# Optimization experiments

Hardware: AMD Instinct MI355X
Metric: run time of the kernel (lower is better)

## Reference

```python
import jax, jax.numpy as jnp
import numpy as np

D = 256; H = 8; DK = 32; L = 5; FF = 2048; K = 31
EPS_LN = 1e-12  # espnet LayerNorm eps
EPS_BN = 1e-5   # torch BatchNorm1d eps


def _ln(x, g, b):
    mu = x.mean(-1, keepdims=True)
    v = ((x - mu) ** 2).mean(-1, keepdims=True)
    return (x - mu) / jnp.sqrt(v + EPS_LN) * g + b


def _swish(x):
    return x * jax.nn.sigmoid(x)


def _pos_emb(T):
    # espnet RelPositionalEncoding: relative positions T-1 .. -(T-1), length 2T-1
    pos = jnp.arange(T, dtype=jnp.float32)[:, None]
    div = jnp.exp(jnp.arange(0, D, 2, dtype=jnp.float32) * (-np.log(10000.0) / D))[None, :]
    pe_pos = jnp.stack([jnp.sin(pos * div), jnp.cos(pos * div)], -1).reshape(T, D)
    pe_neg = jnp.stack([jnp.sin(-pos * div), jnp.cos(-pos * div)], -1).reshape(T, D)
    return jnp.concatenate([pe_pos[::-1], pe_neg[1:]], 0)  # (2T-1, D)


def _rel_shift(x):
    # x: (B, H, T, 2T-1) -> (B, H, T, T), Transformer-XL style shift
    B, Hh, T, N = x.shape
    x = jnp.pad(x, ((0, 0), (0, 0), (0, 0), (1, 0)))
    x = x.reshape(B, Hh, N + 1, T)[:, :, 1:, :].reshape(B, Hh, T, N)
    return x[..., : (N // 2 + 1)]


def _attn(x, pe, mask, Wq, bq, Wk, bk, Wv, bv, Wo, bo, Wp, pu, pv):
    B, T, _ = x.shape
    q = (x @ Wq.T + bq).reshape(B, T, H, DK)
    k = (x @ Wk.T + bk).reshape(B, T, H, DK).transpose(0, 2, 1, 3)
    v = (x @ Wv.T + bv).reshape(B, T, H, DK).transpose(0, 2, 1, 3)
    p = (pe @ Wp.T).reshape(-1, H, DK)  # (2T-1, H, DK)
    qu = (q + pu).transpose(0, 2, 1, 3)
    qv = (q + pv).transpose(0, 2, 1, 3)
    ac = jnp.einsum('bhtd,bhsd->bhts', qu, k)
    bd = _rel_shift(jnp.einsum('bhtd,nhd->bhtn', qv, p))
    scores = (ac + bd) / np.sqrt(DK)
    m = mask[:, None, :, :]  # (B,1,1,T)
    scores = jnp.where(m, scores, -1e30)
    a = jax.nn.softmax(scores, -1)
    a = jnp.where(m, a, 0.0)
    out = jnp.einsum('bhts,bhsd->bthd', a, v).reshape(B, T, D)
    return out @ Wo.T + bo


def _conv(x, pw1_w, pw1_b, dw_w, dw_b, bn_g, bn_b, pw2_w, pw2_b):
    y = x @ pw1_w.T + pw1_b                      # (B,T,2D)
    a, b = jnp.split(y, 2, -1)
    y = (a * jax.nn.sigmoid(b)).transpose(0, 2, 1)  # GLU -> (B,D,T)
    y = jax.lax.conv_general_dilated(
        y, dw_w[:, None, :], (1,), [(K // 2, K // 2)],
        feature_group_count=D, dimension_numbers=('NCW', 'OIW', 'NCW')
    ) + dw_b[None, :, None]
    mu = y.mean((0, 2), keepdims=True)
    var = ((y - mu) ** 2).mean((0, 2), keepdims=True)  # batch stats (train mode)
    y = (y - mu) / jnp.sqrt(var + EPS_BN) * bn_g[None, :, None] + bn_b[None, :, None]
    y = _swish(y).transpose(0, 2, 1)
    return y @ pw2_w.T + pw2_b


def _forward(xs, Wemb, bemb, ln_in_g, ln_in_b, Wq, bq, Wk, bk, Wv, bv, Wo, bo, Wp,
             pos_u, pos_v, ln1_g, ln1_b, lnc_g, lnc_b, lnf_g, lnf_b, lnfin_g, lnfin_b,
             pw1_w, pw1_b, dw_w, dw_b, bn_g, bn_b, pw2_w, pw2_b,
             ff1_w, ff1_b, ff2_w, ff2_b, after_g, after_b, mask):
    B, T, _ = xs.shape
    x = _ln(xs @ Wemb.T + bemb, ln_in_g, ln_in_b)  # linear input layer + LN
    x = x * np.sqrt(D)                              # rel-pos encoding x-scale
    pe = _pos_emb(T)
    for i in range(L):
        x = x + _attn(_ln(x, ln1_g[i], ln1_b[i]), pe, mask,
                      Wq[i], bq[i], Wk[i], bk[i], Wv[i], bv[i], Wo[i], bo[i],
                      Wp[i], pos_u[i], pos_v[i])
        x = x + _conv(_ln(x, lnc_g[i], lnc_b[i]),
                      pw1_w[i], pw1_b[i], dw_w[i], dw_b[i],
                      bn_g[i], bn_b[i], pw2_w[i], pw2_b[i])
        h = _ln(x, lnf_g[i], lnf_b[i])
        x = x + _swish(h @ ff1_w[i].T + ff1_b[i]) @ ff2_w[i].T + ff2_b[i]
        x = _ln(x, lnfin_g[i], lnfin_b[i])
    x = _ln(x, after_g, after_b)
    return x.sum(1)  # (B, D) sum-pool over time


def setup_inputs() -> dict:
    key = jax.random.key(0)
    ks = iter(jax.random.split(key, 32))
    B, T, IDIM = 8, 1024, 80
    nrm = lambda shp: jax.random.normal(next(ks), shp, jnp.float32) * 0.02
    z = lambda shp: jnp.zeros(shp, jnp.float32)
    o = lambda shp: jnp.ones(shp, jnp.float32)
    return {
        'xs': jax.random.normal(next(ks), (B, T, IDIM), jnp.float32),
        'Wemb': nrm((D, IDIM)), 'bemb': z((D,)),
        'ln_in_g': o((D,)), 'ln_in_b': z((D,)),
        'Wq': nrm((L, D, D)), 'bq': z((L, D)),
        'Wk': nrm((L, D, D)), 'bk': z((L, D)),
        'Wv': nrm((L, D, D)), 'bv': z((L, D)),
        'Wo': nrm((L, D, D)), 'bo': z((L, D)),
        'Wp': nrm((L, D, D)),
        'pos_u': nrm((L, H, DK)), 'pos_v': nrm((L, H, DK)),
        'ln1_g': o((L, D)), 'ln1_b': z((L, D)),
        'lnc_g': o((L, D)), 'lnc_b': z((L, D)),
        'lnf_g': o((L, D)), 'lnf_b': z((L, D)),
        'lnfin_g': o((L, D)), 'lnfin_b': z((L, D)),
        'pw1_w': nrm((L, 2 * D, D)), 'pw1_b': z((L, 2 * D)),
        'dw_w': nrm((L, D, K)), 'dw_b': z((L, D)),
        'bn_g': o((L, D)), 'bn_b': z((L, D)),
        'pw2_w': nrm((L, D, D)), 'pw2_b': z((L, D)),
        'ff1_w': nrm((L, FF, D)), 'ff1_b': z((L, FF)),
        'ff2_w': nrm((L, D, FF)), 'ff2_b': z((L, D)),
        'after_g': o((D,)), 'after_b': z((D,)),
        'mask': jnp.ones((B, 1, T), bool),
    }


def reference(xs, Wemb, bemb, ln_in_g, ln_in_b, Wq, bq, Wk, bk, Wv, bv, Wo, bo, Wp,
              pos_u, pos_v, ln1_g, ln1_b, lnc_g, lnc_b, lnf_g, lnf_b, lnfin_g, lnfin_b,
              pw1_w, pw1_b, dw_w, dw_b, bn_g, bn_b, pw2_w, pw2_b,
              ff1_w, ff1_b, ff2_w, ff2_b, after_g, after_b, mask):
    return _forward(xs, Wemb, bemb, ln_in_g, ln_in_b, Wq, bq, Wk, bk, Wv, bv, Wo, bo, Wp,
                    pos_u, pos_v, ln1_g, ln1_b, lnc_g, lnc_b, lnf_g, lnf_b, lnfin_g, lnfin_b,
                    pw1_w, pw1_b, dw_w, dw_b, bn_g, bn_b, pw2_w, pw2_b,
                    ff1_w, ff1_b, ff2_w, ff2_b, after_g, after_b, mask)
```

## Files before the change

### kernel.cpp

```cpp
#include <hip/hip_runtime.h>
#include <math.h>


#define Bq 8
#define Tq 1024
#define Dq 256
#define Hq 8
#define FFq 2048
#define IDIMq 80
#define ROWS (Bq * Tq)
#define NPOS (2 * Tq - 1)

typedef _Float16 half8 __attribute__((ext_vector_type(8)));
typedef _Float16 half4v __attribute__((ext_vector_type(4)));
typedef _Float16 half2v __attribute__((ext_vector_type(2)));
typedef float floatx4 __attribute__((ext_vector_type(4)));

__device__ __forceinline__ float sigm(float x) { return 1.f / (1.f + __expf(-x)); }

__device__ __forceinline__ float wave_sum64(float v) {
    #pragma unroll
    for (int off = 1; off < 64; off <<= 1) v += __shfl_xor(v, off, 64);
    return v;
}

__device__ __forceinline__ void load_lds16(const _Float16* g, _Float16* l) {
    __builtin_amdgcn_global_load_lds(
        (const __attribute__((address_space(1))) void*)g,
        (__attribute__((address_space(3))) void*)l, 16, 0, 0);
}

__global__ void k_f2h(const float* __restrict__ in, _Float16* __restrict__ out, int n4) {
    int i = blockIdx.x * 256 + threadIdx.x;
    if (i < n4) {
        float4 v = ((const float4*)in)[i];
        half4v h; h[0] = (_Float16)v.x; h[1] = (_Float16)v.y; h[2] = (_Float16)v.z; h[3] = (_Float16)v.w;
        ((half4v*)out)[i] = h;
    }
}

__global__ void k_pack_qkv(const float* __restrict__ Wq, const float* __restrict__ Wk,
                           const float* __restrict__ Wv, const float* __restrict__ bq,
                           const float* __restrict__ bk, const float* __restrict__ bv,
                           _Float16* __restrict__ WH, float* __restrict__ BH) {
    int i = blockIdx.x * 256 + threadIdx.x;
    if (i >= 5 * 768 * 64) return;
    int c4 = i & 63;
    int row = (i >> 6) % 768;
    int l = i / (768 * 64);
    int sect = row >> 8, r = row & 255;
    const float* W = sect == 0 ? Wq : (sect == 1 ? Wk : Wv);
    float4 v = *(const float4*)(W + ((size_t)l * 256 + r) * 256 + c4 * 4);
    half4v h; h[0] = (_Float16)v.x; h[1] = (_Float16)v.y; h[2] = (_Float16)v.z; h[3] = (_Float16)v.w;
    *(half4v*)(WH + ((size_t)l * 768 + row) * 256 + c4 * 4) = h;
    if (c4 == 0) {
        const float* bsrc = sect == 0 ? bq : (sect == 1 ? bk : bv);
        BH[l * 768 + row] = bsrc[l * 256 + r];
    }
}

__global__ void k_wtrans(const float* __restrict__ dw_w, float* __restrict__ WT) {
    int l = blockIdx.x, c = threadIdx.x;
    for (int k = 0; k < 31; ++k)
        WT[((size_t)l * 31 + k) * 256 + c] = dw_w[((size_t)l * 256 + c) * 31 + k];
}

__global__ void k_pe(_Float16* __restrict__ PE) {
    int n = blockIdx.x;
    int d = threadIdx.x;
    int i = d >> 1;
    double div = exp(-(double)(2 * i) * log(10000.0) / 256.0);
    double arg = (double)(1023 - n) * div;
    float v = (d & 1) ? (float)cos(arg) : (float)sin(arg);
    PE[(size_t)n * Dq + d] = (_Float16)v;
}

__global__ __launch_bounds__(256) void k_embed_mm(
    const float* __restrict__ xs, const float* __restrict__ Wemb,
    const float* __restrict__ bemb, float* __restrict__ E) {
    __shared__ float xr[8][IDIMq];
    const int tid = threadIdx.x;
    const int r0 = blockIdx.x * 8;
    for (int idx = tid; idx < 8 * IDIMq; idx += 256) {
        int r = idx / IDIMq, c = idx % IDIMq;
        xr[r][c] = xs[(size_t)(r0 + r) * IDIMq + c];
    }
    __syncthreads();
    float4 w[20];
    const float4* wp = (const float4*)(Wemb + (size_t)tid * IDIMq);
    #pragma unroll
    for (int i = 0; i < 20; ++i) w[i] = wp[i];
    const float bias = bemb[tid];
    #pragma unroll
    for (int r = 0; r < 8; ++r) {
        float acc = bias;
        const float* x = xr[r];
        #pragma unroll
        for (int i = 0; i < 20; ++i)
            acc += w[i].x * x[4 * i] + w[i].y * x[4 * i + 1]
                 + w[i].z * x[4 * i + 2] + w[i].w * x[4 * i + 3];
        E[(size_t)(r0 + r) * 256 + tid] = acc;
    }
}

__global__ __launch_bounds__(256) void k_lnw(
    const float* __restrict__ Xin, const float* __restrict__ g,
    const float* __restrict__ bb, _Float16* __restrict__ O) {
    const int lane = threadIdx.x & 63;
    const int row = blockIdx.x * 4 + (threadIdx.x >> 6);
    const float4 v = *(const float4*)(Xin + (size_t)row * 256 + lane * 4);
    float mu = wave_sum64(v.x + v.y + v.z + v.w) * (1.f / 256.f);
    float dx = v.x - mu, dy = v.y - mu, dz = v.z - mu, dw = v.w - mu;
    float var = wave_sum64(dx * dx + dy * dy + dz * dz + dw * dw) * (1.f / 256.f);
    float rstd = 1.f / sqrtf(var + 1e-12f);
    const float4 gg = *(const float4*)(g + lane * 4);
    const float4 bv = *(const float4*)(bb + lane * 4);
    half4v o;
    o[0] = (_Float16)(dx * rstd * gg.x + bv.x);
    o[1] = (_Float16)(dy * rstd * gg.y + bv.y);
    o[2] = (_Float16)(dz * rstd * gg.z + bv.z);
    o[3] = (_Float16)(dw * rstd * gg.w + bv.w);
    *(half4v*)(O + (size_t)row * 256 + lane * 4) = o;
}

__global__ __launch_bounds__(256) void k_ln2w(
    const float* __restrict__ Xin, const float* __restrict__ g1,
    const float* __restrict__ b1, float s1,
    const float* __restrict__ g2, const float* __restrict__ b2,
    float* __restrict__ Xout, _Float16* __restrict__ XH) {
    const int lane = threadIdx.x & 63;
    const int row = blockIdx.x * 4 + (threadIdx.x >> 6);
    const float4 v = *(const float4*)(Xin + (size_t)row * 256 + lane * 4);
    float mu = wave_sum64(v.x + v.y + v.z + v.w) * (1.f / 256.f);
    float dx = v.x - mu, dy = v.y - mu, dz = v.z - mu, dw = v.w - mu;
    float var = wave_sum64(dx * dx + dy * dy + dz * dz + dw * dw) * (1.f / 256.f);
    float rstd = 1.f / sqrtf(var + 1e-12f);
    const float4 g1v = *(const float4*)(g1 + lane * 4);
    const float4 b1v = *(const float4*)(b1 + lane * 4);
    float4 y;
    y.x = (dx * rstd * g1v.x + b1v.x) * s1;
    y.y = (dy * rstd * g1v.y + b1v.y) * s1;
    y.z = (dz * rstd * g1v.z + b1v.z) * s1;
    y.w = (dw * rstd * g1v.w + b1v.w) * s1;
    *(float4*)(Xout + (size_t)row * 256 + lane * 4) = y;
    float mu2 = wave_sum64(y.x + y.y + y.z + y.w) * (1.f / 256.f);
    float ex = y.x - mu2, ey = y.y - mu2, ez = y.z - mu2, ew = y.w - mu2;
    float var2 = wave_sum64(ex * ex + ey * ey + ez * ez + ew * ew) * (1.f / 256.f);
    float rstd2 = 1.f / sqrtf(var2 + 1e-12f);
    const float4 g2v = *(const float4*)(g2 + lane * 4);
    const float4 b2v = *(const float4*)(b2 + lane * 4);
    half4v o;
    o[0] = (_Float16)(ex * rstd2 * g2v.x + b2v.x);
    o[1] = (_Float16)(ey * rstd2 * g2v.y + b2v.y);
    o[2] = (_Float16)(ez * rstd2 * g2v.z + b2v.z);
    o[3] = (_Float16)(ew * rstd2 * g2v.w + b2v.w);
    *(half4v*)(XH + (size_t)row * 256 + lane * 4) = o;
}

#define GF_SWISH 1
#define GF_ACC   2
#define GF_F16   4
#define GF_PH    8
#define GF_BNA   16
#define GF_QKV   32
template<int KC, int TM>
__global__ __launch_bounds__(256) void k_gemm2(
    const _Float16* __restrict__ A, const _Float16* __restrict__ W,
    const float* __restrict__ bias, const float* __restrict__ bnp,
    float* __restrict__ Cf, _Float16* __restrict__ Ch,
    int M, int N, int ldw, int woff, int flags) {
    constexpr int NF = TM / 32;
    const int tid = threadIdx.x;
    const int wave = tid >> 6, lane = tid & 63;
    const int quad = lane >> 4, l16 = lane & 15;
    const int m0 = blockIdx.y * TM + (wave & 1) * (TM / 2);
    const int n0 = blockIdx.x * 64 + (wave >> 1) * 32;
    const _Float16* Ap[NF];
    #pragma unroll
    for (int i = 0; i < NF; ++i) {
        int r_ = m0 + 16 * i + l16;
        if (r_ >= M) r_ = M - 1;
        Ap[i] = A + (size_t)r_ * KC + quad * 8;
    }
    const _Float16* Wp0 = W + (size_t)(n0 + l16) * ldw + woff + quad * 8;
    const _Float16* Wp1 = Wp0 + (size_t)16 * ldw;
    floatx4 acc[NF][2] = {};
    for (int ko = 0; ko < KC; ko += 256) {
        #pragma unroll
        for (int k1 = 0; k1 < 256 && k1 < KC; k1 += 32) {
            int k0 = ko + k1;
            half8 b0 = *(const half8*)(Wp0 + k0);
            half8 b1 = *(const half8*)(Wp1 + k0);
            float scv[8], shv[8];
            if (flags & GF_BNA) {
                *(float4*)&scv[0] = *(const float4*)(bnp + k0 + quad * 8);
                *(float4*)&scv[4] = *(const float4*)(bnp + k0 + quad * 8 + 4);
                *(float4*)&shv[0] = *(const float4*)(bnp + 256 + k0 + quad * 8);
                *(float4*)&shv[4] = *(const float4*)(bnp + 256 + k0 + quad * 8 + 4);
            }
            #pragma unroll
            for (int i = 0; i < NF; ++i) {
                half8 a = *(const half8*)(Ap[i] + k0);
                if (flags & GF_BNA) {
                    #pragma unroll
                    for (int j = 0; j < 8; ++j) {
                        float f = (float)a[j] * scv[j] + shv[j];
                        a[j] = (_Float16)(f * sigm(f));
                    }
                }
                acc[i][0] = __builtin_amdgcn_mfma_f32_16x16x32_f16(a, b0, acc[i][0], 0, 0, 0);
                acc[i][1] = __builtin_amdgcn_mfma_f32_16x16x32_f16(a, b1, acc[i][1], 0, 0, 0);
            }
        }
    }
    #pragma unroll
    for (int i = 0; i < NF; ++i) {
        #pragma unroll
        for (int j = 0; j < 2; ++j) {
            #pragma unroll
            for (int r = 0; r < 4; ++r) {
                int row = m0 + i * 16 + quad * 4 + r;
                int col = n0 + j * 16 + l16;
                if (row < M) {
                    float v = acc[i][j][r];
                    if (bias) v += bias[col];
                    if (flags & GF_SWISH) v = v * sigm(v);
                    if (flags & GF_PH) {
                        Ch[((size_t)(col >> 5) * 2048 + row) * 32 + (col & 31)] = (_Float16)v;
                    } else {
                        size_t idx = (size_t)row * N + col;
                        if (flags & GF_ACC) Cf[idx] += v;
                        else if (flags & GF_F16) Ch[idx] = (_Float16)v;
                        else Cf[idx] = v;
                    }
                }
            }
        }
    }
}

template<int KC>
__global__ __launch_bounds__(256, 2) void k_gemm4(
    const _Float16* __restrict__ A, const _Float16* __restrict__ W,
    const float* __restrict__ bias, _Float16* __restrict__ Ch,
    int M, int N, int flags) {
    __shared__ _Float16 As[128 * 32];
    __shared__ _Float16 Bs[128 * 32];
    const int tid = threadIdx.x;
    const int wave = tid >> 6, lane = tid & 63;
    const int quad = lane >> 4, l16 = lane & 15;
    const int m0 = blockIdx.y * 128, n0 = blockIdx.x * 128;
    const int wm = (wave & 1) * 64, wn = (wave >> 1) * 64;
    const int r4 = lane >> 2;
    const int c4 = (lane & 3) * 8;
    const _Float16* Ag0 = A + (size_t)(m0 + wave * 32 + r4) * KC + c4;
    const _Float16* Ag1 = Ag0 + (size_t)16 * KC;
    const _Float16* Wg0 = W + (size_t)(n0 + wave * 32 + r4) * KC + c4;
    const _Float16* Wg1 = Wg0 + (size_t)16 * KC;
    _Float16* la0 = As + (wave * 32) * 32;
    _Float16* la1 = As + (wave * 32 + 16) * 32;
    _Float16* lb0 = Bs + (wave * 32) * 32;
    _Float16* lb1 = Bs + (wave * 32 + 16) * 32;
    floatx4 acc[4][4] = {};
    for (int k0 = 0; k0 < KC; k0 += 32) {
        __syncthreads();
        load_lds16(Ag0 + k0, la0);
        load_lds16(Ag1 + k0, la1);
        load_lds16(Wg0 + k0, lb0);
        load_lds16(Wg1 + k0, lb1);
        __syncthreads();
        half8 bfr[4];
        #pragma unroll
        for (int j = 0; j < 4; ++j)
            bfr[j] = *(const half8*)(Bs + (wn + 16 * j + l16) * 32 + quad * 8);
        #pragma unroll
        for (int i = 0; i < 4; ++i) {
            half8 a = *(const half8*)(As + (wm + 16 * i + l16) * 32 + quad * 8);
            acc[i][0] = __builtin_amdgcn_mfma_f32_16x16x32_f16(a, bfr[0], acc[i][0], 0, 0, 0);
            acc[i][1] = __builtin_amdgcn_mfma_f32_16x16x32_f16(a, bfr[1], acc[i][1], 0, 0, 0);
            acc[i][2] = __builtin_amdgcn_mfma_f32_16x16x32_f16(a, bfr[2], acc[i][2], 0, 0, 0);
            acc[i][3] = __builtin_amdgcn_mfma_f32_16x16x32_f16(a, bfr[3], acc[i][3], 0, 0, 0);
        }
    }
    #pragma unroll
    for (int i = 0; i < 4; ++i) {
        #pragma unroll
        for (int j = 0; j < 4; ++j) {
            #pragma unroll
            for (int r = 0; r < 4; ++r) {
                int row = m0 + wm + i * 16 + quad * 4 + r;
                int col = n0 + wn + j * 16 + l16;
                float v = acc[i][j][r];
                if (bias) v += bias[col];
                if (flags & GF_SWISH) v = v * sigm(v);
                if (flags & GF_QKV) {
                    if (col < 256) {
                        Ch[(size_t)row * 256 + col] = (_Float16)v;
                    } else if (col < 512) {
                        int hh = (col - 256) >> 5, d = col & 31;
                        int bb2 = row >> 10, t = row & 1023;
                        Ch[2097152 + (((size_t)(bb2 * 8 + hh) << 10) + t) * 32 + d] = (_Float16)v;
                    } else {
                        Ch[4194304 + (size_t)row * 256 + (col - 512)] = (_Float16)v;
                    }
                } else {
                    Ch[(size_t)row * N + col] = (_Float16)v;
                }
            }
        }
    }
}

__global__ __launch_bounds__(256) void k_gemm_glu(
    const _Float16* __restrict__ A, const _Float16* __restrict__ W,
    const float* __restrict__ bias, _Float16* __restrict__ Oh) {
    const int tid = threadIdx.x;
    const int wave = tid >> 6, lane = tid & 63;
    const int quad = lane >> 4, l16 = lane & 15;
    const int m0 = blockIdx.y * 128 + (wave & 1) * 64;
    const int n0 = blockIdx.x * 64 + (wave >> 1) * 32;
    const int K = 256;
    const _Float16* Ap[4];
    #pragma unroll
    for (int i = 0; i < 4; ++i)
        Ap[i] = A + (size_t)(m0 + 16 * i + l16) * K + quad * 8;
    const _Float16* Wa0 = W + (size_t)(n0 + l16) * K + quad * 8;
    const _Float16* Wa1 = Wa0 + (size_t)16 * K;
    const _Float16* Wb0 = Wa0 + (size_t)256 * K;
    const _Float16* Wb1 = Wa1 + (size_t)256 * K;
    floatx4 acc1[4][2] = {}, acc2[4][2] = {};
    #pragma unroll
    for (int k0 = 0; k0 < 256; k0 += 32) {
        half8 b0 = *(const half8*)(Wa0 + k0);
        half8 b1 = *(const half8*)(Wa1 + k0);
        half8 c0 = *(const half8*)(Wb0 + k0);
        half8 c1 = *(const half8*)(Wb1 + k0);
        #pragma unroll
        for (int i = 0; i < 4; ++i) {
            half8 a = *(const half8*)(Ap[i] + k0);
            acc1[i][0] = __builtin_amdgcn_mfma_f32_16x16x32_f16(a, b0, acc1[i][0], 0, 0, 0);
            acc1[i][1] = __builtin_amdgcn_mfma_f32_16x16x32_f16(a, b1, acc1[i][1], 0, 0, 0);
            acc2[i][0] = __builtin_amdgcn_mfma_f32_16x16x32_f16(a, c0, acc2[i][0], 0, 0, 0);
            acc2[i][1] = __builtin_amdgcn_mfma_f32_16x16x32_f16(a, c1, acc2[i][1], 0, 0, 0);
        }
    }
    #pragma unroll
    for (int i = 0; i < 4; ++i) {
        #pragma unroll
        for (int j = 0; j < 2; ++j) {
            #pragma unroll
            for (int r = 0; r < 4; ++r) {
                int row = m0 + i * 16 + quad * 4 + r;
                int col = n0 + j * 16 + l16;
                float a = acc1[i][j][r] + bias[col];
                float g = acc2[i][j][r] + bias[256 + col];
                Oh[(size_t)row * 256 + col] = (_Float16)(a * sigm(g));
            }
        }
    }
}

__global__ __launch_bounds__(256) void k_vtrans(const _Float16* __restrict__ VH,
                                                _Float16* __restrict__ VT) {
    __shared__ _Float16 S[64][264];
    const int r0 = blockIdx.x * 64;
    const int b = r0 >> 10;
    const int tid = threadIdx.x;
    #pragma unroll
    for (int i = 0; i < 8; ++i) {
        int idx = tid + 256 * i;
        int row = idx >> 5, ch = idx & 31;
        uint4 v = *(const uint4*)(VH + (size_t)(r0 + row) * 256 + ch * 8);
        *(uint4*)(&S[row][ch * 8]) = v;
    }
    __syncthreads();
    const int s0 = r0 & 1023;
    _Float16* dst = VT + ((size_t)(b * 8) * 32 + (tid >> 5) * 32 + (tid & 31)) * 1024 + s0;
    #pragma unroll
    for (int p0 = 0; p0 < 64; p0 += 8) {
        half8 t;
        #pragma unroll
        for (int j = 0; j < 8; ++j) {
            int pos = p0 + j;
            int blk = pos >> 5, pl = pos & 31;
            int srow = blk * 32 + (pl >> 1) + 16 * (pl & 1);
            t[j] = S[srow][tid];
        }
        *(half8*)(dst + p0) = t;
    }
}

__global__ __launch_bounds__(256, 4) void k_attn7(
    const _Float16* __restrict__ QH, const _Float16* __restrict__ KH,
    const _Float16* __restrict__ PH, const _Float16* __restrict__ VT,
    const float* __restrict__ pu, const float* __restrict__ pv,
    _Float16* __restrict__ Out) {
    __shared__ __align__(16) _Float16 Pl[4][16 * 40];
    const int tid = threadIdx.x;
    const int wave = tid >> 6, lane = tid & 63;
    const int quad = lane >> 4, l16 = lane & 15;
    const int h = blockIdx.y, b = blockIdx.z;
    const int tb = blockIdx.x * 64 + wave * 16;
    const float scale = 0.17677669529663687f;
    half8 qu_f, qv_f;
    {
        half8 q = *(const half8*)(QH + ((size_t)(b * Tq) + tb + l16) * 256 + h * 32 + quad * 8);
        #pragma unroll
        for (int j = 0; j < 8; ++j) {
            float qf = (float)q[j];
            qu_f[j] = (_Float16)((qf + pu[h * 32 + quad * 8 + j]) * scale);
            qv_f[j] = (_Float16)((qf + pv[h * 32 + quad * 8 + j]) * scale);
        }
    }
    int srcA[4];
    bool selA[4], selB[4];
    #pragma unroll
    for (int r = 0; r < 4; ++r) {
        int tt = quad * 4 + r;
        int cp0 = l16 - tt + 15;
        srcA[r] = quad * 16 + (cp0 & 15);
        selA[r] = (cp0 >> 4) != 0;
        selB[r] = ((cp0 + 16) >> 4) != 1;
    }
    floatx4 o0 = {0.f, 0.f, 0.f, 0.f}, o1 = {0.f, 0.f, 0.f, 0.f};
    float l_r[4] = {0.f, 0.f, 0.f, 0.f};
    const _Float16* Kbase = KH + ((size_t)(b * 8 + h) << 10) * 32 + quad * 8;
    const _Float16* Vbase = VT + ((size_t)(b * 8 + h) * 32 + l16) * 1024 + quad * 8;
    const _Float16* Pbase = PH + (size_t)h * 2048 * 32 + quad * 8;
    const int nb0 = 1023 - tb - 15;
    _Float16* plH = &Pl[wave][0];
    unsigned int* plU = (unsigned int*)plH;
    half8 vb0, vb1;
    floatx4 sc0, sc1, d0, d1, d2;
    {
        half8 kb0 = *(const half8*)(Kbase + (size_t)l16 * 32);
        half8 kb1 = *(const half8*)(Kbase + (size_t)(16 + l16) * 32);
        half8 pb0 = *(const half8*)(Pbase + (size_t)(nb0 + l16) * 32);
        half8 pb1 = *(const half8*)(Pbase + (size_t)(nb0 + 16 + l16) * 32);
        half8 pb2 = *(const half8*)(Pbase + (size_t)(nb0 + 32 + l16) * 32);
        vb0 = *(const half8*)(Vbase);
        vb1 = *(const half8*)(Vbase + 16 * 1024);
        floatx4 z = {0.f, 0.f, 0.f, 0.f};
        sc0 = __builtin_amdgcn_mfma_f32_16x16x32_f16(qu_f, kb0, z, 0, 0, 0);
        sc1 = __builtin_amdgcn_mfma_f32_16x16x32_f16(qu_f, kb1, z, 0, 0, 0);
        d0 = __builtin_amdgcn_mfma_f32_16x16x32_f16(qv_f, pb0, z, 0, 0, 0);
        d1 = __builtin_amdgcn_mfma_f32_16x16x32_f16(qv_f, pb1, z, 0, 0, 0);
        d2 = __builtin_amdgcn_mfma_f32_16x16x32_f16(qv_f, pb2, z, 0, 0, 0);
    }
    for (int it = 0; it < 32; ++it) {
        const int sbn = (it == 31) ? it * 32 : (it + 1) * 32;
        half8 nk0 = *(const half8*)(Kbase + (size_t)(sbn + l16) * 32);
        half8 nk1 = *(const half8*)(Kbase + (size_t)(sbn + 16 + l16) * 32);
        half8 np0 = *(const half8*)(Pbase + (size_t)(nb0 + sbn + l16) * 32);
        half8 np1 = *(const half8*)(Pbase + (size_t)(nb0 + sbn + 16 + l16) * 32);
        half8 np2 = *(const half8*)(Pbase + (size_t)(nb0 + sbn + 32 + l16) * 32);
        half8 nv0 = *(const half8*)(Vbase + sbn);
        half8 nv1 = *(const half8*)(Vbase + 16 * 1024 + sbn);
        #pragma unroll
        for (int r = 0; r < 4; ++r) {
            half2v pk01; pk01[0] = (_Float16)d0[r]; pk01[1] = (_Float16)d1[r];
            half2v pk12; pk12[0] = (_Float16)d1[r]; pk12[1] = (_Float16)d2[r];
            float gA = __shfl(__builtin_bit_cast(float, pk01), srcA[r]);
            float gB = __shfl(__builtin_bit_cast(float, pk12), srcA[r]);
            half2v hA = __builtin_bit_cast(half2v, gA);
            half2v hB = __builtin_bit_cast(half2v, gB);
            float bd0 = (float)(selA[r] ? hA[1] : hA[0]);
            float bd1 = (float)(selB[r] ? hB[1] : hB[0]);
            float p0 = __expf(sc0[r] + bd0);
            float p1 = __expf(sc1[r] + bd1);
            l_r[r] += p0 + p1;
            half2v pp; pp[0] = (_Float16)p0; pp[1] = (_Float16)p1;
            plU[(quad * 4 + r) * 20 + l16] = __builtin_bit_cast(unsigned int, pp);
        }
        floatx4 z = {0.f, 0.f, 0.f, 0.f};
        floatx4 t0 = __builtin_amdgcn_mfma_f32_16x16x32_f16(qu_f, nk0, z, 0, 0, 0);
        floatx4 t1 = __builtin_amdgcn_mfma_f32_16x16x32_f16(qu_f, nk1, z, 0, 0, 0);
        floatx4 t2 = __builtin_amdgcn_mfma_f32_16x16x32_f16(qv_f, np0, z, 0, 0, 0);
        floatx4 t3 = __builtin_amdgcn_mfma_f32_16x16x32_f16(qv_f, np1, z, 0, 0, 0);
        floatx4 t4 = __builtin_amdgcn_mfma_f32_16x16x32_f16(qv_f, np2, z, 0, 0, 0);
        half4v lo = *(const half4v*)(plH + l16 * 40 + quad * 8);
        half4v hi = *(const half4v*)(plH + l16 * 40 + quad * 8 + 4);
        half8 pa;
        pa[0] = lo[0]; pa[1] = lo[1]; pa[2] = lo[2]; pa[3] = lo[3];
        pa[4] = hi[0]; pa[5] = hi[1]; pa[6] = hi[2]; pa[7] = hi[3];
        o0 = __builtin_amdgcn_mfma_f32_16x16x32_f16(pa, vb0, o0, 0, 0, 0);
        o1 = __builtin_amdgcn_mfma_f32_16x16x32_f16(pa, vb1, o1, 0, 0, 0);
        sc0 = t0; sc1 = t1; d0 = t2; d1 = t3; d2 = t4;
        vb0 = nv0; vb1 = nv1;
    }
    #pragma unroll
    for (int r = 0; r < 4; ++r) {
        float l = l_r[r];
        #pragma unroll
        for (int off = 1; off < 16; off <<= 1) l += __shfl_xor(l, off);
        float inv = 1.f / l;
        size_t ob = ((size_t)(b * Tq) + tb + quad * 4 + r) * 256 + h * 32;
        Out[ob + l16] = (_Float16)(o0[r] * inv);
        Out[ob + 16 + l16] = (_Float16)(o1[r] * inv);
    }
}

__global__ __launch_bounds__(256) void k_dwconv4(
    const _Float16* __restrict__ Xin, const float* __restrict__ WT,
    const float* __restrict__ wb, _Float16* __restrict__ Y,
    float* __restrict__ SP, float* __restrict__ SP2) {
    __shared__ float spb[4][256], sp2b[4][256];
    const int tid = threadIdx.x;
    const int cg = tid & 63;
    const int strip = tid >> 6;
    const int row0 = blockIdx.x * 32 + strip * 8;
    const int t0 = row0 & 1023;
    const int c4 = cg * 4;
    const _Float16* xb = Xin + (size_t)(row0 - t0) * 256 + c4;
    float4 bias = *(const float4*)(wb + c4);
    float4 acc[8];
    #pragma unroll
    for (int j = 0; j < 8; ++j) acc[j] = bias;
    float4 win[8];
    #pragma unroll
    for (int j = 0; j < 8; ++j) {
        int t = t0 - 15 + j;
        if (t >= 0 && t < Tq) {
            half4v x = *(const half4v*)(xb + (size_t)t * 256);
            win[j] = make_float4((float)x[0], (float)x[1], (float)x[2], (float)x[3]);
        } else win[j] = make_float4(0.f, 0.f, 0.f, 0.f);
    }
    #pragma unroll
    for (int k = 0; k < 31; ++k) {
        float4 wk = *(const float4*)(WT + (size_t)k * 256 + c4);
        #pragma unroll
        for (int j = 0; j < 8; ++j) {
            acc[j].x += wk.x * win[j].x;
            acc[j].y += wk.y * win[j].y;
            acc[j].z += wk.z * win[j].z;
            acc[j].w += wk.w * win[j].w;
        }
        if (k < 30) {
            int t = t0 - 7 + k;
            float4 nw;
            if (t >= 0 && t < Tq) {
                half4v x = *(const half4v*)(xb + (size_t)t * 256);
                nw = make_float4((float)x[0], (float)x[1], (float)x[2], (float)x[3]);
            } else nw = make_float4(0.f, 0.f, 0.f, 0.f);
            #pragma unroll
            for (int j = 0; j < 7; ++j) win[j] = win[j + 1];
            win[7] = nw;
        }
    }
    float4 s = make_float4(0.f, 0.f, 0.f, 0.f), s2 = make_float4(0.f, 0.f, 0.f, 0.f);
    #pragma unroll
    for (int j = 0; j < 8; ++j) {
        half4v o; o[0] = (_Float16)acc[j].x; o[1] = (_Float16)acc[j].y;
        o[2] = (_Float16)acc[j].z; o[3] = (_Float16)acc[j].w;
        *(half4v*)(Y + (size_t)(row0 + j) * 256 + c4) = o;
        s.x += acc[j].x; s.y += acc[j].y; s.z += acc[j].z; s.w += acc[j].w;
        s2.x += acc[j].x * acc[j].x; s2.y += acc[j].y * acc[j].y;
        s2.z += acc[j].z * acc[j].z; s2.w += acc[j].w * acc[j].w;
    }
    *(float4*)&spb[strip][c4] = s;
    *(float4*)&sp2b[strip][c4] = s2;
    __syncthreads();
    if (tid < 256) {
        SP[blockIdx.x * 256 + tid] = spb[0][tid] + spb[1][tid] + spb[2][tid] + spb[3][tid];
        SP2[blockIdx.x * 256 + tid] = sp2b[0][tid] + sp2b[1][tid] + sp2b[2][tid] + sp2b[3][tid];
    }
}

__global__ void k_bns2(const float* __restrict__ SP, const float* __restrict__ SP2,
                       const float* __restrict__ g, const float* __restrict__ bb,
                       float* __restrict__ BNS) {
    int c = blockIdx.x;
    int p = threadIdx.x;
    __shared__ float rs[256], rs2[256];
    rs[p] = SP[p * 256 + c];
    rs2[p] = SP2[p * 256 + c];
    __syncthreads();
    for (int st = 128; st > 0; st >>= 1) {
        if (p < st) { rs[p] += rs[p + st]; rs2[p] += rs2[p + st]; }
        __syncthreads();
    }
    if (p == 0) {
        float mu = rs[0] / (float)ROWS;
        float var = rs2[0] / (float)ROWS - mu * mu;
        float rstd = 1.f / sqrtf(var + 1e-5f);
        float sc = rstd * g[c];
        BNS[c] = sc;
        BNS[256 + c] = bb[c] - mu * sc;
    }
}

__global__ void k_partial(const _Float16* __restrict__ Xl, float* __restrict__ Pt) {
    int chunk = blockIdx.x, b = blockIdx.y, d = threadIdx.x;
    float s = 0.f;
    int t0 = chunk * 32;
    for (int t = 0; t < 32; ++t)
        s += (float)Xl[((size_t)b * Tq + t0 + t) * Dq + d];
    Pt[((size_t)b * 32 + chunk) * Dq + d] = s;
}
__global__ void k_finalsum(const float* __restrict__ Pt, float* __restrict__ out) {
    int b = blockIdx.x, d = threadIdx.x;
    float s = 0.f;
    for (int c = 0; c < 32; ++c)
        s += Pt[((size_t)b * 32 + c) * Dq + d];
    out[(size_t)b * Dq + d] = s;
}

extern "C" void kernel_launch(void* const* d_in, const int* in_sizes, int n_in,
                              void* d_out, int out_size, void* d_ws, size_t ws_size,
                              hipStream_t stream) {
    const float* xs      = (const float*)d_in[0];
    const float* Wemb    = (const float*)d_in[1];
    const float* bemb    = (const float*)d_in[2];
    const float* ln_in_g = (const float*)d_in[3];
    const float* ln_in_b = (const float*)d_in[4];
    const float* Wq      = (const float*)d_in[5];
    const float* bq      = (const float*)d_in[6];
    const float* Wk      = (const float*)d_in[7];
    const float* bk      = (const float*)d_in[8];
    const float* Wv      = (const float*)d_in[9];
    const float* bv      = (const float*)d_in[10];
    const float* Wo      = (const float*)d_in[11];
    const float* bo      = (const float*)d_in[12];
    const float* Wp      = (const float*)d_in[13];
    const float* pos_u   = (const float*)d_in[14];
    const float* pos_v   = (const float*)d_in[15];
    const float* ln1_g   = (const float*)d_in[16];
    const float* ln1_b   = (const float*)d_in[17];
    const float* lnc_g   = (const float*)d_in[18];
    const float* lnc_b   = (const float*)d_in[19];
    const float* lnf_g   = (const float*)d_in[20];
    const float* lnf_b   = (const float*)d_in[21];
    const float* lnfin_g = (const float*)d_in[22];
    const float* lnfin_b = (const float*)d_in[23];
    const float* pw1_w   = (const float*)d_in[24];
    const float* pw1_b   = (const float*)d_in[25];
    const float* dw_w    = (const float*)d_in[26];
    const float* dw_b    = (const float*)d_in[27];
    const float* bn_g    = (const float*)d_in[28];
    const float* bn_b    = (const float*)d_in[29];
    const float* pw2_w   = (const float*)d_in[30];
    const float* pw2_b   = (const float*)d_in[31];
    const float* ff1_w   = (const float*)d_in[32];
    const float* ff1_b   = (const float*)d_in[33];
    const float* ff2_w   = (const float*)d_in[34];
    const float* ff2_b   = (const float*)d_in[35];
    const float* after_g = (const float*)d_in[36];
    const float* after_b = (const float*)d_in[37];

    char* wsb = (char*)d_ws;
    const size_t MB = (size_t)1 << 20;
    float*     X    = (float*)(wsb + 0);
    _Float16*  XH   = (_Float16*)(wsb + 8 * MB);
    _Float16*  PEh  = (_Float16*)(wsb + 12 * MB);
    float*     BNS  = (float*)(wsb + 13 * MB);
    float*     SP   = (float*)(wsb + 13 * MB + 4096);
    float*     SP2  = (float*)(wsb + 13 * MB + 4096 + 262144);
    float*     BQKV = (float*)(wsb + 13 * MB + 4096 + 524288);
    float*     PART = (float*)(wsb + 13 * MB + 4096 + 524288 + 16384);
    float*     WT   = (float*)(wsb + 13 * MB + 4096 + 524288 + 16384 + 262144);
    _Float16*  WH   = (_Float16*)(wsb + 14 * MB);
    _Float16*  QKVd = (_Float16*)(wsb + 30 * MB);
    _Float16*  T1h  = (_Float16*)(wsb + 42 * MB);
    _Float16*  T2h  = (_Float16*)(wsb + 46 * MB);
    float*     E    = (float*)(wsb + 42 * MB);
    _Float16*  FFHh = (_Float16*)(wsb + 30 * MB);
    _Float16*  PHp  = (_Float16*)(wsb + 50 * MB);
    _Float16*  VT   = (_Float16*)(wsb + 51 * MB);

    _Float16*  QH   = QKVd;
    _Float16*  KH   = QKVd + 2097152;
    _Float16*  VH   = QKVd + 4194304;

    _Float16* WoH   = WH;
    _Float16* WpH   = WH + 327680;
    _Float16* pw1H  = WH + 655360;
    _Float16* pw2H  = WH + 1310720;
    _Float16* ff1H  = WH + 1638400;
    _Float16* ff2H  = WH + 4259840;
    _Float16* WqkvH = WH + 6881280;

    auto f2h = [&](const float* in, _Float16* out, size_t n) {
        int n4 = (int)(n >> 2);
        k_f2h<<<dim3((n4 + 255) / 256), dim3(256), 0, stream>>>(in, out, n4);
    };

    f2h(Wo, WoH, 5 * 65536);
    f2h(Wp, WpH, 5 * 65536);
    f2h(pw1_w, pw1H, 5 * 131072);
    f2h(pw2_w, pw2H, 5 * 65536);
    f2h(ff1_w, ff1H, (size_t)5 * 524288);
    f2h(ff2_w, ff2H, (size_t)5 * 524288);
    k_pack_qkv<<<dim3(960), dim3(256), 0, stream>>>(Wq, Wk, Wv, bq, bk, bv, WqkvH, BQKV);
    k_wtrans<<<dim3(5), dim3(256), 0, stream>>>(dw_w, WT);
    k_pe<<<dim3(NPOS), dim3(256), 0, stream>>>(PEh);
    k_embed_mm<<<dim3(ROWS / 8), dim3(256), 0, stream>>>(xs, Wemb, bemb, E);
    k_ln2w<<<dim3(ROWS / 4), dim3(256), 0, stream>>>(
        E, ln_in_g, ln_in_b, 16.f, ln1_g, ln1_b, X, XH);

    for (int l = 0; l < 5; ++l) {
        k_gemm4<256><<<dim3(6, 64), dim3(256), 0, stream>>>(
            XH, WqkvH + (size_t)l * 196608, BQKV + l * 768, QKVd, ROWS, 768, GF_QKV);
        k_gemm2<256, 128><<<dim3(4, 16), dim3(256), 0, stream>>>(
            PEh, WpH + (size_t)l * 65536, nullptr, nullptr, nullptr, PHp,
            NPOS, 256, 256, 0, GF_F16 | GF_PH);
        k_vtrans<<<dim3(ROWS / 64), dim3(256), 0, stream>>>(VH, VT);
        k_attn7<<<dim3(Tq / 64, Hq, Bq), dim3(256), 0, stream>>>(
            QH, KH, PHp, VT, pos_u + l * Dq, pos_v + l * Dq, T1h);
        k_gemm2<256, 64><<<dim3(4, 128), dim3(256), 0, stream>>>(
            T1h, WoH + (size_t)l * 65536, bo + l * Dq, nullptr, X, nullptr,
            ROWS, 256, 256, 0, GF_ACC);
        k_lnw<<<dim3(ROWS / 4), dim3(256), 0, stream>>>(X, lnc_g + l * Dq, lnc_b + l * Dq, XH);
        k_gemm_glu<<<dim3(4, ROWS / 128), dim3(256), 0, stream>>>(
            XH, pw1H + (size_t)l * 131072, pw1_b + l * 512, T1h);
        k_dwconv4<<<dim3(ROWS / 32), dim3(256), 0, stream>>>(
            T1h, WT + (size_t)l * 31 * 256, dw_b + l * Dq, T2h, SP, SP2);
        k_bns2<<<dim3(256), dim3(256), 0, stream>>>(SP, SP2, bn_g + l * Dq, bn_b + l * Dq, BNS);
        k_gemm2<256, 64><<<dim3(4, 128), dim3(256), 0, stream>>>(
            T2h, pw2H + (size_t)l * 65536, pw2_b + l * Dq, BNS, X, nullptr,
            ROWS, 256, 256, 0, GF_ACC | GF_BNA);
        k_lnw<<<dim3(ROWS / 4), dim3(256), 0, stream>>>(X, lnf_g + l * Dq, lnf_b + l * Dq, XH);
        const _Float16* f1 = ff1H + (size_t)l * 524288;
        const _Float16* f2 = ff2H + (size_t)l * 524288;
        k_gemm4<256><<<dim3(8, 64), dim3(256), 0, stream>>>(
            XH, f1, ff1_b + l * FFq, FFHh, ROWS, 1024, GF_SWISH | GF_F16);
        k_gemm2<1024, 64><<<dim3(4, 128), dim3(256), 0, stream>>>(
            FFHh, f2, ff2_b + l * Dq, nullptr, X, nullptr,
            ROWS, 256, 2048, 0, GF_ACC);
        k_gemm4<256><<<dim3(8, 64), dim3(256), 0, stream>>>(
            XH, f1 + (size_t)1024 * 256, ff1_b + l * FFq + 1024, FFHh, ROWS, 1024,
            GF_SWISH | GF_F16);
        k_gemm2<1024, 64><<<dim3(4, 128), dim3(256), 0, stream>>>(
            FFHh, f2, nullptr, nullptr, X, nullptr,
            ROWS, 256, 2048, 1024, GF_ACC);
        const float* g2 = (l < 4) ? (ln1_g + (l + 1) * Dq) : after_g;
        const float* b2 = (l < 4) ? (ln1_b + (l + 1) * Dq) : after_b;
        k_ln2w<<<dim3(ROWS / 4), dim3(256), 0, stream>>>(
            X, lnfin_g + l * Dq, lnfin_b + l * Dq, 1.f, g2, b2, X, XH);
    }

    k_partial<<<dim3(32, Bq), dim3(256), 0, stream>>>(XH, PART);
    k_finalsum<<<dim3(Bq), dim3(256), 0, stream>>>(PART, (float*)d_out);
}
```

Baseline: 1.783 ms.

## Add LDS-staged 64x64 GEMM kernel for residual-accumulating projections

Adds a new GEMM kernel that stages 64x32 tiles of A and W into shared memory, using the existing load_lds16 helper, before feeding MFMA. Each wave computes a 32x32 sub-tile from the shared tiles instead of reading A and W directly from global memory. The BN+swish prologue moves into the new kernel and is removed from k_gemm2. The new kernel replaces k_gemm2 for the Wo, pw2 and both FF2 half GEMMs. It is meant to reuse loaded data across waves and cut redundant global loads, but it adds two barriers per 32-wide K step and has no double buffering.

```diff
diff --git a/kernel.cpp b/kernel.cpp
--- a/kernel.cpp
+++ b/kernel.cpp
@@ -191,23 +191,9 @@
             int k0 = ko + k1;
             half8 b0 = *(const half8*)(Wp0 + k0);
             half8 b1 = *(const half8*)(Wp1 + k0);
-            float scv[8], shv[8];
-            if (flags & GF_BNA) {
-                *(float4*)&scv[0] = *(const float4*)(bnp + k0 + quad * 8);
-                *(float4*)&scv[4] = *(const float4*)(bnp + k0 + quad * 8 + 4);
-                *(float4*)&shv[0] = *(const float4*)(bnp + 256 + k0 + quad * 8);
-                *(float4*)&shv[4] = *(const float4*)(bnp + 256 + k0 + quad * 8 + 4);
-            }
             #pragma unroll
             for (int i = 0; i < NF; ++i) {
                 half8 a = *(const half8*)(Ap[i] + k0);
-                if (flags & GF_BNA) {
-                    #pragma unroll
-                    for (int j = 0; j < 8; ++j) {
-                        float f = (float)a[j] * scv[j] + shv[j];
-                        a[j] = (_Float16)(f * sigm(f));
-                    }
-                }
                 acc[i][0] = __builtin_amdgcn_mfma_f32_16x16x32_f16(a, b0, acc[i][0], 0, 0, 0);
                 acc[i][1] = __builtin_amdgcn_mfma_f32_16x16x32_f16(a, b1, acc[i][1], 0, 0, 0);
             }
@@ -306,6 +292,69 @@
                 } else {
                     Ch[(size_t)row * N + col] = (_Float16)v;
                 }
+            }
+        }
+    }
+}
+
+template<int KC>
+__global__ __launch_bounds__(256, 2) void k_gemm5(
+    const _Float16* __restrict__ A, const _Float16* __restrict__ W,
+    const float* __restrict__ bias, const float* __restrict__ bnp,
+    float* __restrict__ Cf, int M, int N, int ldw, int woff, int flags) {
+    __shared__ _Float16 As[64 * 32];
+    __shared__ _Float16 Bs[64 * 32];
+    const int tid = threadIdx.x;
+    const int wave = tid >> 6, lane = tid & 63;
+    const int quad = lane >> 4, l16 = lane & 15;
+    const int m0 = blockIdx.y * 64, n0 = blockIdx.x * 64;
+    const int wm = (wave & 1) * 32, wn = (wave >> 1) * 32;
+    const int r4 = lane >> 2;
+    const int c4 = (lane & 3) * 8;
+    const _Float16* Ag = A + (size_t)(m0 + wave * 16 + r4) * KC + c4;
+    const _Float16* Wg = W + (size_t)(n0 + wave * 16 + r4) * ldw + woff + c4;
+    _Float16* la = As + (wave * 16) * 32;
+    _Float16* lb = Bs + (wave * 16) * 32;
+    floatx4 acc[2][2] = {};
+    for (int k0 = 0; k0 < KC; k0 += 32) {
+        __syncthreads();
+        load_lds16(Ag + k0, la);
+        load_lds16(Wg + k0, lb);
+        __syncthreads();
+        half8 a0 = *(const half8*)(As + (wm + l16) * 32 + quad * 8);
+        half8 a1 = *(const half8*)(As + (wm + 16 + l16) * 32 + quad * 8);
+        half8 b0 = *(const half8*)(Bs + (wn + l16) * 32 + quad * 8);
+        half8 b1 = *(const half8*)(Bs + (wn + 16 + l16) * 32 + quad * 8);
+        if (flags & GF_BNA) {
+            float scv[8], shv[8];
+            *(float4*)&scv[0] = *(const float4*)(bnp + k0 + quad * 8);
+            *(float4*)&scv[4] = *(const float4*)(bnp + k0 + quad * 8 + 4);
+            *(float4*)&shv[0] = *(const float4*)(bnp + 256 + k0 + quad * 8);
+            *(float4*)&shv[4] = *(const float4*)(bnp + 256 + k0 + quad * 8 + 4);
+            #pragma unroll
+            for (int j = 0; j < 8; ++j) {
+                float f0 = (float)a0[j] * scv[j] + shv[j];
+                float f1 = (float)a1[j] * scv[j] + shv[j];
+                a0[j] = (_Float16)(f0 * sigm(f0));
+                a1[j] = (_Float16)(f1 * sigm(f1));
+            }
+        }
+        acc[0][0] = __builtin_amdgcn_mfma_f32_16x16x32_f16(a0, b0, acc[0][0], 0, 0, 0);
+        acc[0][1] = __builtin_amdgcn_mfma_f32_16x16x32_f16(a0, b1, acc[0][1], 0, 0, 0);
+        acc[1][0] = __builtin_amdgcn_mfma_f32_16x16x32_f16(a1, b0, acc[1][0], 0, 0, 0);
+        acc[1][1] = __builtin_amdgcn_mfma_f32_16x16x32_f16(a1, b1, acc[1][1], 0, 0, 0);
+    }
+    #pragma unroll
+    for (int i = 0; i < 2; ++i) {
+        #pragma unroll
+        for (int j = 0; j < 2; ++j) {
+            #pragma unroll
+            for (int r = 0; r < 4; ++r) {
+                int row = m0 + wm + i * 16 + quad * 4 + r;
+                int col = n0 + wn + j * 16 + l16;
+                float v = acc[i][j][r];
+                if (bias) v += bias[col];
+                Cf[(size_t)row * N + col] += v;
             }
         }
     }
@@ -706,8 +755,8 @@
         k_vtrans<<<dim3(ROWS / 64), dim3(256), 0, stream>>>(VH, VT);
         k_attn7<<<dim3(Tq / 64, Hq, Bq), dim3(256), 0, stream>>>(
             QH, KH, PHp, VT, pos_u + l * Dq, pos_v + l * Dq, T1h);
-        k_gemm2<256, 64><<<dim3(4, 128), dim3(256), 0, stream>>>(
-            T1h, WoH + (size_t)l * 65536, bo + l * Dq, nullptr, X, nullptr,
+        k_gemm5<256><<<dim3(4, 128), dim3(256), 0, stream>>>(
+            T1h, WoH + (size_t)l * 65536, bo + l * Dq, nullptr, X,
             ROWS, 256, 256, 0, GF_ACC);
         k_lnw<<<dim3(ROWS / 4), dim3(256), 0, stream>>>(X, lnc_g + l * Dq, lnc_b + l * Dq, XH);
         k_gemm_glu<<<dim3(4, ROWS / 128), dim3(256), 0, stream>>>(
@@ -715,22 +764,22 @@
         k_dwconv4<<<dim3(ROWS / 32), dim3(256), 0, stream>>>(
             T1h, WT + (size_t)l * 31 * 256, dw_b + l * Dq, T2h, SP, SP2);
         k_bns2<<<dim3(256), dim3(256), 0, stream>>>(SP, SP2, bn_g + l * Dq, bn_b + l * Dq, BNS);
-        k_gemm2<256, 64><<<dim3(4, 128), dim3(256), 0, stream>>>(
-            T2h, pw2H + (size_t)l * 65536, pw2_b + l * Dq, BNS, X, nullptr,
+        k_gemm5<256><<<dim3(4, 128), dim3(256), 0, stream>>>(
+            T2h, pw2H + (size_t)l * 65536, pw2_b + l * Dq, BNS, X,
             ROWS, 256, 256, 0, GF_ACC | GF_BNA);
         k_lnw<<<dim3(ROWS / 4), dim3(256), 0, stream>>>(X, lnf_g + l * Dq, lnf_b + l * Dq, XH);
         const _Float16* f1 = ff1H + (size_t)l * 524288;
         const _Float16* f2 = ff2H + (size_t)l * 524288;
         k_gemm4<256><<<dim3(8, 64), dim3(256), 0, stream>>>(
             XH, f1, ff1_b + l * FFq, FFHh, ROWS, 1024, GF_SWISH | GF_F16);
-        k_gemm2<1024, 64><<<dim3(4, 128), dim3(256), 0, stream>>>(
-            FFHh, f2, ff2_b + l * Dq, nullptr, X, nullptr,
+        k_gemm5<1024><<<dim3(4, 128), dim3(256), 0, stream>>>(
+            FFHh, f2, ff2_b + l * Dq, nullptr, X,
             ROWS, 256, 2048, 0, GF_ACC);
         k_gemm4<256><<<dim3(8, 64), dim3(256), 0, stream>>>(
             XH, f1 + (size_t)1024 * 256, ff1_b + l * FFq + 1024, FFHh, ROWS, 1024,
             GF_SWISH | GF_F16);
-        k_gemm2<1024, 64><<<dim3(4, 128), dim3(256), 0, stream>>>(
-            FFHh, f2, nullptr, nullptr, X, nullptr,
+        k_gemm5<1024><<<dim3(4, 128), dim3(256), 0, stream>>>(
+            FFHh, f2, nullptr, nullptr, X,
             ROWS, 256, 2048, 1024, GF_ACC);
         const float* g2 = (l < 4) ? (ln1_g + (l + 1) * Dq) : after_g;
         const float* b2 = (l < 4) ? (ln1_b + (l + 1) * Dq) : after_b;
```

Measured after the change: 1.603 ms. 10.1% less time.
